# Kernel tuning notes

Hardware: AMD Instinct MI355X
Metric: run time of the kernel (lower is better)

The kernel has to match this reference:

```python
import jax, jax.numpy as jnp
import numpy as np

D_MODEL = 1024
LOW_RANK = 128
SCALE = 1.0 / np.sqrt(LOW_RANK)


def _xavier(key, fan_out, fan_in):
    # xavier_uniform for a Linear weight of shape [fan_out, fan_in]
    limit = np.sqrt(6.0 / (fan_in + fan_out))
    return jax.random.uniform(key, (fan_out, fan_in), jnp.float32, -limit, limit)


def setup_inputs() -> dict:
    key = jax.random.key(0)
    k_tgt, k_mem, kq, kk, kv, ko = jax.random.split(key, 6)
    tgt = jax.random.normal(k_tgt, (4, 2048, D_MODEL), jnp.float32)
    memory = jax.random.normal(k_mem, (4, 2048, D_MODEL), jnp.float32)
    Wq = _xavier(kq, LOW_RANK, D_MODEL)   # query_proj.weight
    Wk = _xavier(kk, LOW_RANK, D_MODEL)   # key_proj.weight
    Wv = _xavier(kv, D_MODEL, D_MODEL)    # value_proj.weight
    Wo = _xavier(ko, D_MODEL, D_MODEL)    # out_proj.weight
    return {"tgt": tgt, "memory": memory, "Wq": Wq, "Wk": Wk, "Wv": Wv, "Wo": Wo}


def reference(tgt, memory, Wq, Wk, Wv, Wo):
    # q: [B, T, r], k: [B, S, r], v: [B, S, d]
    q = jnp.einsum('btd,rd->btr', tgt, Wq)
    k = jnp.einsum('bsd,rd->bsr', memory, Wk)
    v = jnp.einsum('bsd,ed->bse', memory, Wv)
    scores = jnp.einsum('btr,bsr->bts', q, k) * SCALE  # [B, T, S]
    attn = jax.nn.softmax(scores, axis=-1)
    # dropout is identity in eval mode
    attn_out = jnp.einsum('bts,bse->bte', attn, v)     # [B, T, d]
    return jnp.einsum('bte,oe->bto', attn_out, Wo)
```

## Files before the change

kernel.cpp:

```cpp
#include <hip/hip_runtime.h>
#include <hip/hip_bf16.h>

#define B_SZ 4
#define T_SZ 2048
#define S_SZ 2048
#define D_SZ 1024
#define R_SZ 128
#define SCALE_F 0.08838834764831845f

typedef __attribute__((ext_vector_type(8))) short short8;
typedef __attribute__((ext_vector_type(4))) float f32x4;
typedef __attribute__((ext_vector_type(4))) float float4v;
typedef __attribute__((ext_vector_type(4))) unsigned short u16x4;

__device__ __forceinline__ unsigned short f2bf(float f) {
  unsigned int u = __float_as_uint(f);
  unsigned int r = (u + 0x7FFFu + ((u >> 16) & 1u)) >> 16;
  return (unsigned short)r;
}

__device__ __forceinline__ void gload_lds16(const unsigned short* g, unsigned short* l) {
  __builtin_amdgcn_global_load_lds(
      (const __attribute__((address_space(1))) unsigned int*)g,
      (__attribute__((address_space(3))) unsigned int*)l, 16, 0, 0);
}

__global__ __launch_bounds__(256) void cvt_f32_bf16_x2(
    const float* __restrict__ a, const float* __restrict__ b,
    unsigned short* __restrict__ oa, unsigned short* __restrict__ ob, int n4) {
  const float* src = blockIdx.z ? b : a;
  unsigned short* dst = blockIdx.z ? ob : oa;
  int i = blockIdx.x * blockDim.x + threadIdx.x;
  int stride = gridDim.x * blockDim.x;
  for (; i < n4; i += stride) {
    float4v v = reinterpret_cast<const float4v*>(src)[i];
    u16x4 o;
    o.x = f2bf(v.x); o.y = f2bf(v.y); o.z = f2bf(v.z); o.w = f2bf(v.w);
    reinterpret_cast<u16x4*>(dst)[i] = o;
  }
}

template <int EPI, int SWZ>
__device__ __forceinline__ void gemm_core(
    const unsigned short* __restrict__ A,
    const unsigned short* __restrict__ B,
    void* __restrict__ Cv, float* __restrict__ lsum,
    int K, int lda, int ldb, int ldc, int bzs,
    long long sA, long long sB, long long sC,
    int GX, int GY, int GZ) {
  __shared__ unsigned short sAB[2][8192];

  int bx, by, bz;
  if (SWZ == 0) {
    bx = blockIdx.x; by = blockIdx.y; bz = blockIdx.z;
  } else {
    const int cpx = (GX * GY * GZ) >> 3;
    const int lid = ((int)blockIdx.x & 7) * cpx + ((int)blockIdx.x >> 3);
    if (SWZ == 1) {
      bx = lid / (GY * GZ); int r = lid - bx * (GY * GZ); bz = r / GY; by = r - bz * GY;
    } else if (SWZ == 2) {
      by = lid / (GX * GZ); int r = lid - by * (GX * GZ); bz = r / GX; bx = r - bz * GX;
    } else {
      bz = lid / (GX * GY); int r = lid - bz * (GX * GY); by = r / GX; bx = r - by * GX;
    }
  }

  const int t = threadIdx.x;
  const int lane = t & 63;
  const int wid = t >> 6;
  const int wr = wid >> 1, wc = wid & 1;
  const long long m0b = (long long)by * 128;
  const long long n0b = (long long)bx * 128;

  A += (long long)bz * sA;
  B += (long long)(bz >> bzs) * sB;

  const unsigned short* As0 = A + (m0b + (t >> 2)) * (long long)lda + (t & 3) * 8;
  const unsigned short* As1 = As0 + 64LL * lda;
  const unsigned short* Bs0 = B + (n0b + (t >> 2)) * (long long)ldb + (t & 3) * 8;
  const unsigned short* Bs1 = Bs0 + 64LL * ldb;

  const int fr = lane & 15;
  const int ko = (lane >> 4) * 8;

  f32x4 acc[4][4] = {};

  auto stage = [&](int k0, unsigned short* buf) {
    unsigned short* d = buf + wid * 512;
    gload_lds16(As0 + k0, d);
    gload_lds16(As1 + k0, d + 2048);
    gload_lds16(Bs0 + k0, d + 4096);
    gload_lds16(Bs1 + k0, d + 6144);
  };
  auto compute = [&](const unsigned short* buf) {
    const unsigned short* aF = buf + (wr * 64 + fr) * 32 + ko;
    const unsigned short* bF = buf + 4096 + (wc * 64 + fr) * 32 + ko;
    short8 a[4], b[4];
#pragma unroll
    for (int i = 0; i < 4; i++) {
      a[i] = *reinterpret_cast<const short8*>(aF + i * 512);
      b[i] = *reinterpret_cast<const short8*>(bF + i * 512);
    }
#pragma unroll
    for (int mi = 0; mi < 4; mi++)
#pragma unroll
      for (int ni = 0; ni < 4; ni++)
        acc[mi][ni] =
            __builtin_amdgcn_mfma_f32_16x16x32_bf16(a[mi], b[ni], acc[mi][ni], 0, 0, 0);
  };

  stage(0, sAB[0]);
  __syncthreads();
  for (int k0 = 0; k0 < K; k0 += 64) {
    stage(k0 + 32, sAB[1]);
    compute(sAB[0]);
    __syncthreads();
    const int kn = (k0 + 64 < K) ? k0 + 64 : 0;
    stage(kn, sAB[0]);
    compute(sAB[1]);
    __syncthreads();
  }

  const int cr = (lane >> 4) * 4;
  const int cc = lane & 15;

  if (EPI == 2) {
    unsigned short* C = (unsigned short*)Cv + bz * sC;
#pragma unroll
    for (int mi = 0; mi < 4; mi++) {
      float rs[4] = {0.f, 0.f, 0.f, 0.f};
#pragma unroll
      for (int ni = 0; ni < 4; ni++)
#pragma unroll
        for (int r = 0; r < 4; r++) {
          long long row = m0b + wr * 64 + mi * 16 + cr + r;
          long long col = n0b + wc * 64 + ni * 16 + cc;
          float e = __expf(acc[mi][ni][r] * SCALE_F);
          C[row * ldc + col] = f2bf(e);
          rs[r] += e;
        }
#pragma unroll
      for (int r = 0; r < 4; r++) {
#pragma unroll
        for (int off = 1; off < 16; off <<= 1) rs[r] += __shfl_xor(rs[r], off);
        if (cc == 0)
          atomicAdd(&lsum[bz * T_SZ + m0b + wr * 64 + mi * 16 + cr + r], rs[r]);
      }
    }
  } else if (EPI == 3) {
    unsigned short* C = (unsigned short*)Cv + bz * sC;
#pragma unroll
    for (int mi = 0; mi < 4; mi++)
#pragma unroll
      for (int r = 0; r < 4; r++) {
        long long row = m0b + wr * 64 + mi * 16 + cr + r;
        float invl = 1.0f / lsum[bz * T_SZ + row];
#pragma unroll
        for (int ni = 0; ni < 4; ni++) {
          long long col = n0b + wc * 64 + ni * 16 + cc;
          C[row * ldc + col] = f2bf(acc[mi][ni][r] * invl);
        }
      }
  } else {
#pragma unroll
    for (int mi = 0; mi < 4; mi++)
#pragma unroll
      for (int ni = 0; ni < 4; ni++)
#pragma unroll
        for (int r = 0; r < 4; r++) {
          long long row = m0b + wr * 64 + mi * 16 + cr + r;
          long long col = n0b + wc * 64 + ni * 16 + cc;
          float val = acc[mi][ni][r];
          if (EPI == 1) {
            unsigned short* C = (unsigned short*)Cv + bz * sC;
            C[row * ldc + col] = f2bf(val);
          } else {
            float* C = (float*)Cv + bz * sC;
            C[row * ldc + col] = val;
          }
        }
  }
}

#define GEMM_ARGS                                                              \
  const unsigned short *A, const unsigned short *B, void *Cv, float *lsum,     \
      int K, int lda, int ldb, int ldc, int bzs, long long sA, long long sB,   \
      long long sC, int GX, int GY, int GZ
#define GEMM_PASS A, B, Cv, lsum, K, lda, ldb, ldc, bzs, sA, sB, sC, GX, GY, GZ

__global__ __launch_bounds__(256) void gemm_qk(GEMM_ARGS)     { gemm_core<1, 0>(GEMM_PASS); }
__global__ __launch_bounds__(256) void gemm_vt(GEMM_ARGS)     { gemm_core<1, 1>(GEMM_PASS); }
__global__ __launch_bounds__(256) void gemm_scores(GEMM_ARGS) { gemm_core<2, 3>(GEMM_PASS); }
__global__ __launch_bounds__(256) void gemm_pv(GEMM_ARGS)     { gemm_core<3, 1>(GEMM_PASS); }
__global__ __launch_bounds__(256) void gemm_out(GEMM_ARGS)    { gemm_core<0, 2>(GEMM_PASS); }

extern "C" void kernel_launch(void* const* d_in, const int* in_sizes, int n_in,
                              void* d_out, int out_size, void* d_ws, size_t ws_size,
                              hipStream_t stream) {
  const float* tgt = (const float*)d_in[0];
  const float* mem = (const float*)d_in[1];
  const float* Wq  = (const float*)d_in[2];
  const float* Wk  = (const float*)d_in[3];
  const float* Wv  = (const float*)d_in[4];
  const float* Wo  = (const float*)d_in[5];
  float* out = (float*)d_out;

  char* p = (char*)d_ws;
  unsigned short* tgt_b = (unsigned short*)p; p += (size_t)B_SZ * T_SZ * D_SZ * 2;
  unsigned short* mem_b = (unsigned short*)p; p += (size_t)B_SZ * S_SZ * D_SZ * 2;
  unsigned short* wq_b  = (unsigned short*)p; p += (size_t)R_SZ * D_SZ * 2;
  unsigned short* wk_b  = (unsigned short*)p; p += (size_t)R_SZ * D_SZ * 2;
  unsigned short* wv_b  = (unsigned short*)p; p += (size_t)D_SZ * D_SZ * 2;
  unsigned short* wo_b  = (unsigned short*)p; p += (size_t)D_SZ * D_SZ * 2;
  unsigned short* q_b   = (unsigned short*)p; p += (size_t)B_SZ * T_SZ * R_SZ * 2;
  unsigned short* k_b   = (unsigned short*)p; p += (size_t)B_SZ * S_SZ * R_SZ * 2;
  unsigned short* vT_b  = (unsigned short*)p; p += (size_t)B_SZ * D_SZ * S_SZ * 2;
  unsigned short* probs = (unsigned short*)p; p += (size_t)B_SZ * T_SZ * S_SZ * 2;
  float* lsum = (float*)p;                    p += (size_t)B_SZ * T_SZ * 4;

  {
    int n4 = (B_SZ * T_SZ * D_SZ) / 4;
    cvt_f32_bf16_x2<<<dim3(2048, 1, 2), dim3(256), 0, stream>>>(tgt, mem, tgt_b, mem_b, n4);
    int n4w = (R_SZ * D_SZ) / 4;
    cvt_f32_bf16_x2<<<dim3(n4w / 256, 1, 2), dim3(256), 0, stream>>>(Wq, Wk, wq_b, wk_b, n4w);
    int n4v = (D_SZ * D_SZ) / 4;
    cvt_f32_bf16_x2<<<dim3(n4v / 256, 1, 2), dim3(256), 0, stream>>>(Wv, Wo, wv_b, wo_b, n4v);
  }

  dim3 blk(256);

  gemm_qk<<<dim3(1, T_SZ / 128, 2 * B_SZ), blk, 0, stream>>>(
      tgt_b, wq_b, q_b, nullptr, D_SZ, D_SZ, D_SZ, R_SZ, 2,
      (long long)T_SZ * D_SZ, (long long)R_SZ * D_SZ, (long long)T_SZ * R_SZ,
      0, 0, 0);

  gemm_vt<<<dim3((S_SZ / 128) * (D_SZ / 128) * B_SZ), blk, 0, stream>>>(
      wv_b, mem_b, vT_b, nullptr, D_SZ, D_SZ, D_SZ, S_SZ, 0,
      0LL, (long long)S_SZ * D_SZ, (long long)D_SZ * S_SZ,
      S_SZ / 128, D_SZ / 128, B_SZ);

  hipMemsetAsync(lsum, 0, (size_t)B_SZ * T_SZ * 4, stream);

  gemm_scores<<<dim3((S_SZ / 128) * (T_SZ / 128) * B_SZ), blk, 0, stream>>>(
      q_b, k_b, probs, lsum, R_SZ, R_SZ, R_SZ, S_SZ, 0,
      (long long)T_SZ * R_SZ, (long long)S_SZ * R_SZ, (long long)T_SZ * S_SZ,
      S_SZ / 128, T_SZ / 128, B_SZ);

  gemm_pv<<<dim3((D_SZ / 128) * (T_SZ / 128) * B_SZ), blk, 0, stream>>>(
      probs, vT_b, tgt_b, lsum, S_SZ, S_SZ, S_SZ, D_SZ, 0,
      (long long)T_SZ * S_SZ, (long long)D_SZ * S_SZ, (long long)T_SZ * D_SZ,
      D_SZ / 128, T_SZ / 128, B_SZ);

  gemm_out<<<dim3((D_SZ / 128) * (T_SZ / 128) * B_SZ), blk, 0, stream>>>(
      tgt_b, wo_b, out, nullptr, D_SZ, D_SZ, D_SZ, D_SZ, 0,
      (long long)T_SZ * D_SZ, 0LL, (long long)T_SZ * D_SZ,
      D_SZ / 128, T_SZ / 128, B_SZ);
}
```

Before: 258.5 us.

## Fold Wo into Wv and drop the separate output projection GEMM

Precomputes the combined weight Wo·Wv once per call, after a transposing bf16 conversion of Wv. The value projection then produces Wo-projected values directly, so the PV GEMM writes the final fp32 output and the separate output-projection GEMM over B*T rows disappears. This adds a small 1024x1024x1024 GEMM and a transpose kernel, and adds an extra bf16 rounding of the fused weight.

```diff
diff --git a/kernel.cpp b/kernel.cpp
--- a/kernel.cpp
+++ b/kernel.cpp
@@ -23,6 +23,19 @@
   __builtin_amdgcn_global_load_lds(
       (const __attribute__((address_space(1))) unsigned int*)g,
       (__attribute__((address_space(3))) unsigned int*)l, 16, 0, 0);
+}
+
+__global__ __launch_bounds__(256) void cvt_f32_bf16(const float* __restrict__ in,
+                                                    unsigned short* __restrict__ out,
+                                                    int n4) {
+  int i = blockIdx.x * blockDim.x + threadIdx.x;
+  int stride = gridDim.x * blockDim.x;
+  for (; i < n4; i += stride) {
+    float4v v = reinterpret_cast<const float4v*>(in)[i];
+    u16x4 o;
+    o.x = f2bf(v.x); o.y = f2bf(v.y); o.z = f2bf(v.z); o.w = f2bf(v.w);
+    reinterpret_cast<u16x4*>(out)[i] = o;
+  }
 }
 
 __global__ __launch_bounds__(256) void cvt_f32_bf16_x2(
@@ -37,6 +50,30 @@
     u16x4 o;
     o.x = f2bf(v.x); o.y = f2bf(v.y); o.z = f2bf(v.z); o.w = f2bf(v.w);
     reinterpret_cast<u16x4*>(dst)[i] = o;
+  }
+}
+
+__global__ __launch_bounds__(256) void cvt_transpose_bf16(
+    const float* __restrict__ in, unsigned short* __restrict__ outp, int n) {
+  __shared__ float tile[64][65];
+  const int t = threadIdx.x;
+  const int c4 = (t & 15) * 4;
+  const int r0 = t >> 4;
+  const int x0 = blockIdx.x * 64;
+  const int y0 = blockIdx.y * 64;
+#pragma unroll
+  for (int rr = 0; rr < 64; rr += 16) {
+    float4v v = *reinterpret_cast<const float4v*>(&in[(long long)(y0 + r0 + rr) * n + x0 + c4]);
+    tile[r0 + rr][c4] = v.x; tile[r0 + rr][c4 + 1] = v.y;
+    tile[r0 + rr][c4 + 2] = v.z; tile[r0 + rr][c4 + 3] = v.w;
+  }
+  __syncthreads();
+#pragma unroll
+  for (int rr = 0; rr < 64; rr += 16) {
+    u16x4 o;
+    o.x = f2bf(tile[c4][r0 + rr]);     o.y = f2bf(tile[c4 + 1][r0 + rr]);
+    o.z = f2bf(tile[c4 + 2][r0 + rr]); o.w = f2bf(tile[c4 + 3][r0 + rr]);
+    *reinterpret_cast<u16x4*>(&outp[(long long)(x0 + r0 + rr) * n + y0 + c4]) = o;
   }
 }
 
@@ -148,7 +185,7 @@
       }
     }
   } else if (EPI == 3) {
-    unsigned short* C = (unsigned short*)Cv + bz * sC;
+    float* C = (float*)Cv + bz * sC;
 #pragma unroll
     for (int mi = 0; mi < 4; mi++)
 #pragma unroll
@@ -158,7 +195,7 @@
 #pragma unroll
         for (int ni = 0; ni < 4; ni++) {
           long long col = n0b + wc * 64 + ni * 16 + cc;
-          C[row * ldc + col] = f2bf(acc[mi][ni][r] * invl);
+          C[row * ldc + col] = acc[mi][ni][r] * invl;
         }
       }
   } else {
@@ -188,11 +225,11 @@
       long long sC, int GX, int GY, int GZ
 #define GEMM_PASS A, B, Cv, lsum, K, lda, ldb, ldc, bzs, sA, sB, sC, GX, GY, GZ
 
+__global__ __launch_bounds__(256) void gemm_wvo(GEMM_ARGS)    { gemm_core<1, 0>(GEMM_PASS); }
 __global__ __launch_bounds__(256) void gemm_qk(GEMM_ARGS)     { gemm_core<1, 0>(GEMM_PASS); }
-__global__ __launch_bounds__(256) void gemm_vt(GEMM_ARGS)     { gemm_core<1, 1>(GEMM_PASS); }
+__global__ __launch_bounds__(256) void gemm_v2t(GEMM_ARGS)    { gemm_core<1, 1>(GEMM_PASS); }
 __global__ __launch_bounds__(256) void gemm_scores(GEMM_ARGS) { gemm_core<2, 3>(GEMM_PASS); }
-__global__ __launch_bounds__(256) void gemm_pv(GEMM_ARGS)     { gemm_core<3, 1>(GEMM_PASS); }
-__global__ __launch_bounds__(256) void gemm_out(GEMM_ARGS)    { gemm_core<0, 2>(GEMM_PASS); }
+__global__ __launch_bounds__(256) void gemm_pvout(GEMM_ARGS)  { gemm_core<3, 1>(GEMM_PASS); }
 
 extern "C" void kernel_launch(void* const* d_in, const int* in_sizes, int n_in,
                               void* d_out, int out_size, void* d_ws, size_t ws_size,
@@ -210,11 +247,12 @@
   unsigned short* mem_b = (unsigned short*)p; p += (size_t)B_SZ * S_SZ * D_SZ * 2;
   unsigned short* wq_b  = (unsigned short*)p; p += (size_t)R_SZ * D_SZ * 2;
   unsigned short* wk_b  = (unsigned short*)p; p += (size_t)R_SZ * D_SZ * 2;
-  unsigned short* wv_b  = (unsigned short*)p; p += (size_t)D_SZ * D_SZ * 2;
   unsigned short* wo_b  = (unsigned short*)p; p += (size_t)D_SZ * D_SZ * 2;
+  unsigned short* wvT_b = (unsigned short*)p; p += (size_t)D_SZ * D_SZ * 2;
+  unsigned short* wvo_b = (unsigned short*)p; p += (size_t)D_SZ * D_SZ * 2;
   unsigned short* q_b   = (unsigned short*)p; p += (size_t)B_SZ * T_SZ * R_SZ * 2;
   unsigned short* k_b   = (unsigned short*)p; p += (size_t)B_SZ * S_SZ * R_SZ * 2;
-  unsigned short* vT_b  = (unsigned short*)p; p += (size_t)B_SZ * D_SZ * S_SZ * 2;
+  unsigned short* v2T_b = (unsigned short*)p; p += (size_t)B_SZ * D_SZ * S_SZ * 2;
   unsigned short* probs = (unsigned short*)p; p += (size_t)B_SZ * T_SZ * S_SZ * 2;
   float* lsum = (float*)p;                    p += (size_t)B_SZ * T_SZ * 4;
 
@@ -224,18 +262,23 @@
     int n4w = (R_SZ * D_SZ) / 4;
     cvt_f32_bf16_x2<<<dim3(n4w / 256, 1, 2), dim3(256), 0, stream>>>(Wq, Wk, wq_b, wk_b, n4w);
     int n4v = (D_SZ * D_SZ) / 4;
-    cvt_f32_bf16_x2<<<dim3(n4v / 256, 1, 2), dim3(256), 0, stream>>>(Wv, Wo, wv_b, wo_b, n4v);
+    cvt_f32_bf16<<<dim3(n4v / 256), dim3(256), 0, stream>>>(Wo, wo_b, n4v);
+    cvt_transpose_bf16<<<dim3(D_SZ / 64, D_SZ / 64), dim3(256), 0, stream>>>(Wv, wvT_b, D_SZ);
   }
 
   dim3 blk(256);
+
+  gemm_wvo<<<dim3(D_SZ / 128, D_SZ / 128, 1), blk, 0, stream>>>(
+      wo_b, wvT_b, wvo_b, nullptr, D_SZ, D_SZ, D_SZ, D_SZ, 0,
+      0LL, 0LL, 0LL, 0, 0, 0);
 
   gemm_qk<<<dim3(1, T_SZ / 128, 2 * B_SZ), blk, 0, stream>>>(
       tgt_b, wq_b, q_b, nullptr, D_SZ, D_SZ, D_SZ, R_SZ, 2,
       (long long)T_SZ * D_SZ, (long long)R_SZ * D_SZ, (long long)T_SZ * R_SZ,
       0, 0, 0);
 
-  gemm_vt<<<dim3((S_SZ / 128) * (D_SZ / 128) * B_SZ), blk, 0, stream>>>(
-      wv_b, mem_b, vT_b, nullptr, D_SZ, D_SZ, D_SZ, S_SZ, 0,
+  gemm_v2t<<<dim3((S_SZ / 128) * (D_SZ / 128) * B_SZ), blk, 0, stream>>>(
+      wvo_b, mem_b, v2T_b, nullptr, D_SZ, D_SZ, D_SZ, S_SZ, 0,
       0LL, (long long)S_SZ * D_SZ, (long long)D_SZ * S_SZ,
       S_SZ / 128, D_SZ / 128, B_SZ);
 
@@ -246,13 +289,8 @@
       (long long)T_SZ * R_SZ, (long long)S_SZ * R_SZ, (long long)T_SZ * S_SZ,
       S_SZ / 128, T_SZ / 128, B_SZ);
 
-  gemm_pv<<<dim3((D_SZ / 128) * (T_SZ / 128) * B_SZ), blk, 0, stream>>>(
-      probs, vT_b, tgt_b, lsum, S_SZ, S_SZ, S_SZ, D_SZ, 0,
+  gemm_pvout<<<dim3((D_SZ / 128) * (T_SZ / 128) * B_SZ), blk, 0, stream>>>(
+      probs, v2T_b, out, lsum, S_SZ, S_SZ, S_SZ, D_SZ, 0,
       (long long)T_SZ * S_SZ, (long long)D_SZ * S_SZ, (long long)T_SZ * D_SZ,
       D_SZ / 128, T_SZ / 128, B_SZ);
-
-  gemm_out<<<dim3((D_SZ / 128) * (T_SZ / 128) * B_SZ), blk, 0, stream>>>(
-      tgt_b, wo_b, out, nullptr, D_SZ, D_SZ, D_SZ, D_SZ, 0,
-      (long long)T_SZ * D_SZ, 0LL, (long long)T_SZ * D_SZ,
-      D_SZ / 128, T_SZ / 128, B_SZ);
-}
+}
```

Result: faster. 247.3 us (-4.3%).
